# Performance work log

Measured on AMD Instinct MI355X. Metric: run time of the kernel, lower is better.

The kernel has to match this reference:

```python
import jax, jax.numpy as jnp
import numpy as np

HEADS = 8
HEAD_DIM = 32
SCALE = HEAD_DIM ** (-0.5)


def setup_inputs() -> dict:
    key = jax.random.key(0)
    k1, k2, k3 = jax.random.split(key, 3)
    B, DIM, N = 4, 512, 2048
    INNER = HEADS * HEAD_DIM  # 256
    x = jax.random.normal(k1, (B, DIM, N), dtype=jnp.float32)
    # Conv1d(kernel=1, bias=False) == channel-mixing matmul; weight (out_ch, in_ch)
    w_qkv = jax.random.normal(k2, (3 * INNER, DIM), dtype=jnp.float32) * (DIM ** -0.5)
    w_out = jax.random.normal(k3, (DIM, INNER), dtype=jnp.float32) * (INNER ** -0.5)
    b_out = jnp.zeros((DIM,), dtype=jnp.float32)
    return {"x": x, "w_qkv": w_qkv, "w_out": w_out, "b_out": b_out}


def reference(x, w_qkv, w_out, b_out):
    B, DIM, N = x.shape
    INNER = HEADS * HEAD_DIM
    # to_qkv: 1x1 conv over channels, then permute(0,2,1) -> (B, N, 3*INNER)
    qkv = jnp.einsum('bcn,oc->bno', x, w_qkv)
    q, k, v = jnp.split(qkv, 3, axis=-1)
    # 'b n (h d) -> b h n d'
    def to_heads(t):
        return t.reshape(B, N, HEADS, HEAD_DIM).transpose(0, 2, 1, 3)
    q, k, v = to_heads(q), to_heads(k), to_heads(v)
    # L2 similarity: -||q_i - k_j||_2 * scale, via expansion (avoids O(N^2 d) tensor)
    q2 = jnp.sum(q * q, axis=-1)            # (B,H,N)
    k2 = jnp.sum(k * k, axis=-1)            # (B,H,N)
    qk = jnp.einsum('bhid,bhjd->bhij', q, k)  # (B,H,N,N)
    dist2 = q2[..., :, None] + k2[..., None, :] - 2.0 * qk
    smi = -jnp.sqrt(jnp.maximum(dist2, 1e-12)) * SCALE
    attn = jax.nn.softmax(smi, axis=-1)
    out = jnp.einsum('bhij,bhjd->bhid', attn, v)  # (B,H,N,d)
    # 'b h n d -> b (h d) n'
    out = out.transpose(0, 1, 3, 2).reshape(B, INNER, N)
    # to_out: 1x1 conv with bias
    return jnp.einsum('bcn,oc->bon', out, w_out) + b_out[None, :, None]
```

## Files before the change

### kernel.cpp

```cpp
#include <hip/hip_runtime.h>
#include <math.h>

#define N_SEQ 2048
#define DIMC 512
#define INNER 256
#define C2F (0.17677669529663687f * 1.4426950408889634f)
#define C2F2 (C2F * C2F)

typedef short bf16x8 __attribute__((ext_vector_type(8)));
typedef float f32x4 __attribute__((ext_vector_type(4)));


static __device__ __forceinline__ ushort f2bf(float f) {
    uint x = __float_as_uint(f);
    x += 0x7fff + ((x >> 16) & 1);
    return (ushort)(x >> 16);
}
static __device__ __forceinline__ float bf2f(ushort u) {
    return __uint_as_float(((uint)u) << 16);
}
static __device__ __forceinline__ float fast_exp2_neg(float x) {
    float r; asm("v_exp_f32 %0, -%1" : "=v"(r) : "v"(x)); return r;
}
static __device__ __forceinline__ float fast_sqrt(float x) {
    float r; asm("v_sqrt_f32 %0, %1" : "=v"(r) : "v"(x)); return r;
}

__global__ void xpose_cvt(const float* __restrict__ x, ushort* __restrict__ xt) {
    __shared__ __align__(16) ushort T[64][72];
    const int b = blockIdx.z;
    const int c0 = blockIdx.y * 64;
    const int n0 = blockIdx.x * 64;
    const int t = threadIdx.x;
    const int cl = t >> 4;
    const int n4 = (t & 15) * 4;
    const float* xb = x + ((size_t)b * DIMC + c0) * N_SEQ + n0;
#pragma unroll
    for (int cc = 0; cc < 4; ++cc) {
        const int c = cl + cc * 16;
        float4 v = *(const float4*)(xb + (size_t)c * N_SEQ + n4);
        T[n4 + 0][c] = f2bf(v.x);
        T[n4 + 1][c] = f2bf(v.y);
        T[n4 + 2][c] = f2bf(v.z);
        T[n4 + 3][c] = f2bf(v.w);
    }
    __syncthreads();
    const int nl = t >> 2;
    const int c16 = (t & 3) * 16;
    uint4 v0 = *(const uint4*)&T[nl][c16];
    uint4 v1 = *(const uint4*)&T[nl][c16 + 8];
    ushort* dst = xt + ((size_t)b * N_SEQ + n0 + nl) * DIMC + c0 + c16;
    *(uint4*)dst = v0;
    *(uint4*)(dst + 8) = v1;
}

__global__ void wcvt2(const float* __restrict__ wq, const float* __restrict__ wo,
                      ushort* __restrict__ wq16, ushort* __restrict__ wo16) {
    const int bid = blockIdx.x;
    if (bid < 384) {
        int i = (bid * 256 + threadIdx.x) * 4;
        float4 v = *(const float4*)(wq + i);
        ushort4 p;
        p.x = f2bf(v.x); p.y = f2bf(v.y); p.z = f2bf(v.z); p.w = f2bf(v.w);
        *(ushort4*)(wq16 + i) = p;
    } else {
        int i = ((bid - 384) * 256 + threadIdx.x) * 4;
        float4 v = *(const float4*)(wo + i);
        ushort4 p;
        p.x = f2bf(v.x); p.y = f2bf(v.y); p.z = f2bf(v.z); p.w = f2bf(v.w);
        *(ushort4*)(wo16 + i) = p;
    }
}

__global__ __launch_bounds__(256) void qkv_mfma(const ushort* __restrict__ xt,
        const ushort* __restrict__ w16, ushort* __restrict__ ws16) {
    __shared__ __align__(16) ushort Wls[4 * 520];
    __shared__ __align__(16) ushort Xls[4 * 520];
    const int b = blockIdx.z;
    const int o0 = blockIdx.y * 64;
    const int n0 = blockIdx.x * 64;
    const int t = threadIdx.x;
    const int l = t & 63, w = t >> 6;
    const int q15 = l & 15, g = l >> 4;
    f32x4 acc[4];
#pragma unroll
    for (int nn = 0; nn < 4; ++nn) acc[nn] = (f32x4){0.f, 0.f, 0.f, 0.f};
    const int srow = t >> 2, sg = t & 3;
    const ushort* wsrc = w16 + (size_t)(o0 + srow) * DIMC + sg * 8;
    const ushort* xsrc = xt + ((size_t)b * N_SEQ + n0 + srow) * DIMC + sg * 8;
    uint4 wreg = *(const uint4*)wsrc;
    uint4 xreg = *(const uint4*)xsrc;
    for (int k0 = 0; k0 < DIMC; k0 += 32) {
        __builtin_amdgcn_s_barrier();
        __builtin_amdgcn_sched_barrier(0);
        *(uint4*)(Wls + sg * 520 + srow * 8) = wreg;
        *(uint4*)(Xls + sg * 520 + srow * 8) = xreg;
        if (k0 + 32 < DIMC) {
            wreg = *(const uint4*)(wsrc + k0 + 32);
            xreg = *(const uint4*)(xsrc + k0 + 32);
        }
        asm volatile("s_waitcnt lgkmcnt(0)" ::: "memory");
        __builtin_amdgcn_s_barrier();
        __builtin_amdgcn_sched_barrier(0);
        bf16x8 af = *(const bf16x8*)(Wls + g * 520 + (16 * w + q15) * 8);
        __builtin_amdgcn_s_setprio(1);
#pragma unroll
        for (int nn = 0; nn < 4; ++nn) {
            bf16x8 bfr = *(const bf16x8*)(Xls + g * 520 + (16 * nn + q15) * 8);
            acc[nn] = __builtin_amdgcn_mfma_f32_16x16x32_bf16(af, bfr, acc[nn], 0, 0, 0);
        }
        __builtin_amdgcn_s_setprio(0);
    }
    const int oatom = o0 + 16 * w;
    const int t_idx = oatom >> 8;
    const int h = (oatom >> 5) & 7;
    const int bh = b * 8 + h;
    const int d0 = (oatom & 31) + 4 * g;
    if (t_idx < 2) {
        ushort* dst = ws16 + (size_t)t_idx * 2097152 + (size_t)bh * 65536
                      + (size_t)(d0 >> 3) * 16384 + (d0 & 7);
#pragma unroll
        for (int nn = 0; nn < 4; ++nn) {
            const int n_ = n0 + 16 * nn + q15;
            ushort4 p;
            p.x = f2bf(acc[nn][0]); p.y = f2bf(acc[nn][1]);
            p.z = f2bf(acc[nn][2]); p.w = f2bf(acc[nn][3]);
            *(ushort4*)(dst + (size_t)n_ * 8) = p;
        }
    } else {
        ushort* dst = ws16 + (size_t)4194304 + (size_t)bh * 65536;
#pragma unroll
        for (int nn = 0; nn < 4; ++nn) {
            const int n_ = n0 + 16 * nn + q15;
            ushort* dd = dst + (size_t)(n_ >> 3) * 256 + (n_ & 7);
            dd[(d0 + 0) * 8] = f2bf(acc[nn][0]);
            dd[(d0 + 1) * 8] = f2bf(acc[nn][1]);
            dd[(d0 + 2) * 8] = f2bf(acc[nn][2]);
            dd[(d0 + 3) * 8] = f2bf(acc[nn][3]);
        }
    }
}

__global__ void sq_kernel(const ushort* __restrict__ ws16, float* __restrict__ k2) {
    const int idx = blockIdx.x * 256 + threadIdx.x;
    const int bh = idx >> 11, n = idx & 2047;
    const ushort* base = ws16 + 2097152 + (size_t)bh * 65536 + (size_t)n * 8;
    float s = 0.f;
#pragma unroll
    for (int g = 0; g < 4; ++g) {
        uint4 v = *(const uint4*)(base + (size_t)g * 16384);
        uint a[4] = {v.x, v.y, v.z, v.w};
#pragma unroll
        for (int e = 0; e < 4; ++e) {
            float lo = bf2f((ushort)(a[e] & 0xffff));
            float hi = bf2f((ushort)(a[e] >> 16));
            s += lo * lo + hi * hi;
        }
    }
    k2[idx] = s * (float)C2F2;
}

static __device__ __forceinline__ void load_kf(const ushort* __restrict__ Kf,
                                               int jh, bf16x8 (&kf)[4]) {
#pragma unroll
    for (int k = 0; k < 4; ++k)
        kf[k] = *(const bf16x8*)(Kf + (size_t)(jh + 16 * k) * 8);
}

static __device__ __forceinline__ void compute_half(
        const bf16x8 (&kf)[4], const ushort* __restrict__ Vf,
        const float* __restrict__ k2p, int jbase, int half, float q2v,
        bf16x8 qf, bf16x8 onesv, f32x4 (&accO)[2], f32x4& accS,
        ushort* __restrict__ plane, int g) {
    float4 kk[4];
#pragma unroll
    for (int k = 0; k < 4; ++k)
        kk[k] = *(const float4*)(k2p + jbase + half * 64 + 16 * k);
    bf16x8 vfr[4];
#pragma unroll
    for (int jc = 0; jc < 2; ++jc) {
        const int cl = 4 * (2 * half + jc) + g;
        vfr[jc * 2 + 0] = *(const bf16x8*)(Vf + (size_t)jbase * 32 + cl * 256);
        vfr[jc * 2 + 1] = *(const bf16x8*)(Vf + (size_t)jbase * 32 + cl * 256 + 128);
    }
    const f32x4 zz = (f32x4){0.f, 0.f, 0.f, 0.f};
    f32x4 st[4];
    __builtin_amdgcn_s_setprio(1);
#pragma unroll
    for (int k = 0; k < 4; ++k)
        st[k] = __builtin_amdgcn_mfma_f32_16x16x32_bf16(kf[k], qf, zz, 0, 0, 0);
    __builtin_amdgcn_s_setprio(0);
#pragma unroll
    for (int k = 0; k < 4; ++k) {
        float ka[4] = {kk[k].x, kk[k].y, kk[k].z, kk[k].w};
        float pr[4];
#pragma unroll
        for (int r = 0; r < 4; ++r) {
            float a = q2v + ka[r];
            float d2 = fmaf(-2.f * (float)C2F2, st[k][r], a);
            pr[r] = fast_exp2_neg(fast_sqrt(fmaxf(d2, 1e-12f)));
        }
        uint pk0, pk1;
        asm("v_cvt_pk_bf16_f32 %0, %1, %2" : "=v"(pk0) : "v"(pr[0]), "v"(pr[1]));
        asm("v_cvt_pk_bf16_f32 %0, %1, %2" : "=v"(pk1) : "v"(pr[2]), "v"(pr[3]));
        uint2 pv; pv.x = pk0; pv.y = pk1;
        *(uint2*)(plane + 16 * (4 * half + k) + 4 * g) = pv;
    }
    __builtin_amdgcn_s_setprio(1);
#pragma unroll
    for (int jc = 0; jc < 2; ++jc) {
        bf16x8 pf = *(const bf16x8*)(plane + 32 * (2 * half + jc) + 8 * g);
        accO[0] = __builtin_amdgcn_mfma_f32_16x16x32_bf16(vfr[jc * 2 + 0], pf, accO[0], 0, 0, 0);
        accO[1] = __builtin_amdgcn_mfma_f32_16x16x32_bf16(vfr[jc * 2 + 1], pf, accO[1], 0, 0, 0);
        accS = __builtin_amdgcn_mfma_f32_16x16x32_bf16(onesv, pf, accS, 0, 0, 0);
    }
    __builtin_amdgcn_s_setprio(0);
}

__global__ __launch_bounds__(256, 4) void attn_kernel(
        const ushort* __restrict__ ws16, const float* __restrict__ k2g,
        ushort* __restrict__ att16) {
    __shared__ __align__(16) ushort Pls[4][16][140];
    const int bid = blockIdx.x;
    const int sw = (bid & 7) * 128 + (bid >> 3);
    const int q0 = (sw & 31) * 64;
    const int bh = sw >> 5;
    const int b = bh >> 3, h = bh & 7;
    const int tid = threadIdx.x;
    const int l = tid & 63;
    const int w = tid >> 6;
    const int q15 = l & 15;
    const int g = l >> 4;
    const int qrow = q0 + 16 * w + q15;

    const ushort* Qbh = ws16 + (size_t)bh * 65536;
    const ushort* Kf = ws16 + 2097152 + (size_t)bh * 65536
                       + (size_t)g * 16384 + (size_t)q15 * 8;
    const ushort* Vf = ws16 + 4194304 + (size_t)bh * 65536 + (size_t)q15 * 8;
    const float* k2p = k2g + (size_t)bh * 2048 + 4 * g;

    const bf16x8 qf = *(const bf16x8*)(Qbh + (size_t)g * 16384 + (size_t)qrow * 8);
    float q2l = 0.f;
#pragma unroll
    for (int e = 0; e < 8; ++e) {
        float qe = bf2f((ushort)qf[e]);
        q2l = fmaf(qe, qe, q2l);
    }
    q2l += __shfl_xor(q2l, 16);
    q2l += __shfl_xor(q2l, 32);
    const float q2v = q2l * (float)C2F2;

    bf16x8 onesv;
#pragma unroll
    for (int e = 0; e < 8; ++e) onesv[e] = (short)0x3F80;
    ushort* plane = &Pls[w][q15][0];

    f32x4 accO[2];
    accO[0] = (f32x4){0.f, 0.f, 0.f, 0.f};
    accO[1] = (f32x4){0.f, 0.f, 0.f, 0.f};
    f32x4 accS = (f32x4){0.f, 0.f, 0.f, 0.f};

    bf16x8 kfA[4], kfB[4];
    load_kf(Kf, 0, kfA);
    load_kf(Kf, 64, kfB);
#pragma unroll 1
    for (int t = 0; t < 16; ++t) {
        const int jb = t * 128;
        compute_half(kfA, Vf, k2p, jb, 0, q2v, qf, onesv, accO, accS, plane, g);
        load_kf(Kf, jb + 128, kfA);
        __builtin_amdgcn_sched_barrier(0);
        compute_half(kfB, Vf, k2p, jb, 1, q2v, qf, onesv, accO, accS, plane, g);
        load_kf(Kf, jb + 192, kfB);
        __builtin_amdgcn_sched_barrier(0);
    }

    const float invl = 1.f / accS[0];
    ushort* dst = att16 + ((size_t)(b * N_SEQ + qrow)) * INNER + h * 32 + 4 * g;
#pragma unroll
    for (int d = 0; d < 2; ++d) {
        ushort4 o;
        o.x = f2bf(accO[d][0] * invl); o.y = f2bf(accO[d][1] * invl);
        o.z = f2bf(accO[d][2] * invl); o.w = f2bf(accO[d][3] * invl);
        *(ushort4*)(dst + d * 16) = o;
    }
}

__global__ __launch_bounds__(256) void out_mfma(const ushort* __restrict__ att16,
        const ushort* __restrict__ wo16, const float* __restrict__ bias,
        float* __restrict__ out) {
    __shared__ __align__(16) ushort Wls[4 * 520];
    __shared__ __align__(16) ushort Als[4 * 520];
    const int b = blockIdx.z;
    const int o0 = blockIdx.y * 64;
    const int n0 = blockIdx.x * 64;
    const int t = threadIdx.x;
    const int l = t & 63, w = t >> 6;
    const int q15 = l & 15, g = l >> 4;
    f32x4 acc[4];
#pragma unroll
    for (int nn = 0; nn < 4; ++nn) acc[nn] = (f32x4){0.f, 0.f, 0.f, 0.f};
    const int srow = t >> 2, sg = t & 3;
    const ushort* wsrc = wo16 + (size_t)(o0 + srow) * INNER + sg * 8;
    const ushort* asrc = att16 + ((size_t)b * N_SEQ + n0 + srow) * INNER + sg * 8;
    uint4 wreg = *(const uint4*)wsrc;
    uint4 areg = *(const uint4*)asrc;
    for (int k0 = 0; k0 < INNER; k0 += 32) {
        __builtin_amdgcn_s_barrier();
        __builtin_amdgcn_sched_barrier(0);
        *(uint4*)(Wls + sg * 520 + srow * 8) = wreg;
        *(uint4*)(Als + sg * 520 + srow * 8) = areg;
        if (k0 + 32 < INNER) {
            wreg = *(const uint4*)(wsrc + k0 + 32);
            areg = *(const uint4*)(asrc + k0 + 32);
        }
        asm volatile("s_waitcnt lgkmcnt(0)" ::: "memory");
        __builtin_amdgcn_s_barrier();
        __builtin_amdgcn_sched_barrier(0);
        bf16x8 af = *(const bf16x8*)(Wls + g * 520 + (16 * w + q15) * 8);
        __builtin_amdgcn_s_setprio(1);
#pragma unroll
        for (int nn = 0; nn < 4; ++nn) {
            bf16x8 bfr = *(const bf16x8*)(Als + g * 520 + (16 * nn + q15) * 8);
            acc[nn] = __builtin_amdgcn_mfma_f32_16x16x32_bf16(af, bfr, acc[nn], 0, 0, 0);
        }
        __builtin_amdgcn_s_setprio(0);
    }
    const int obase = o0 + 16 * w + 4 * g;
    float4 bi = *(const float4*)(bias + obase);
    float* ob = out + ((size_t)b * DIMC + obase) * N_SEQ;
#pragma unroll
    for (int nn = 0; nn < 4; ++nn) {
        const int n_ = n0 + 16 * nn + q15;
        ob[0 * N_SEQ + n_] = acc[nn][0] + bi.x;
        ob[1 * N_SEQ + n_] = acc[nn][1] + bi.y;
        ob[2 * N_SEQ + n_] = acc[nn][2] + bi.z;
        ob[3 * N_SEQ + n_] = acc[nn][3] + bi.w;
    }
}

extern "C" void kernel_launch(void* const* d_in, const int* in_sizes, int n_in,
                              void* d_out, int out_size, void* d_ws, size_t ws_size,
                              hipStream_t stream) {
    const float* x = (const float*)d_in[0];
    const float* w_qkv = (const float*)d_in[1];
    const float* w_out = (const float*)d_in[2];
    const float* b_out = (const float*)d_in[3];
    ushort* ws16 = (ushort*)d_ws;
    float* k2f = (float*)((char*)d_ws + (12 << 20) + (256 << 10));
    ushort* att16 = (ushort*)((char*)d_ws + (13 << 20));
    ushort* xt16 = (ushort*)((char*)d_ws + (21 << 20));
    ushort* wq16 = (ushort*)((char*)d_ws + (29 << 20));
    ushort* wo16 = (ushort*)((char*)d_ws + (30 << 20));
    float* out = (float*)d_out;

    xpose_cvt<<<dim3(32, 8, 4), 256, 0, stream>>>(x, xt16);
    wcvt2<<<dim3(512), 256, 0, stream>>>(w_qkv, w_out, wq16, wo16);
    qkv_mfma<<<dim3(32, 12, 4), 256, 0, stream>>>(xt16, wq16, ws16);
    sq_kernel<<<dim3(256), 256, 0, stream>>>(ws16, k2f);
    attn_kernel<<<dim3(1024), 256, 0, stream>>>(ws16, k2f, att16);
    out_mfma<<<dim3(32, 8, 4), 256, 0, stream>>>(att16, wo16, b_out, out);
}
```

Before: 91.51 us.

## Software-pipeline QK MFMA one step ahead and compute row sums on VALU

Restructures the attention inner loop so the QK^T MFMAs for the next 64-key chunk are issued while the current chunk's softmax weights are computed and multiplied with V, overlapping matrix and vector work. The softmax denominator is now accumulated in fp32 with VALU adds plus two cross-lane shuffles at the end. This replaces the extra ones-vector MFMA per P-tile. It increases register pressure (next-step st, double-buffered k2 values) and drops the explicit sched barriers. The denominator now sums fp32 weights instead of bf16-rounded ones, so it no longer matches exactly the weights used for P·V.

```diff
diff --git a/kernel.cpp b/kernel.cpp
--- a/kernel.cpp
+++ b/kernel.cpp
@@ -160,63 +160,6 @@
     k2[idx] = s * (float)C2F2;
 }
 
-static __device__ __forceinline__ void load_kf(const ushort* __restrict__ Kf,
-                                               int jh, bf16x8 (&kf)[4]) {
-#pragma unroll
-    for (int k = 0; k < 4; ++k)
-        kf[k] = *(const bf16x8*)(Kf + (size_t)(jh + 16 * k) * 8);
-}
-
-static __device__ __forceinline__ void compute_half(
-        const bf16x8 (&kf)[4], const ushort* __restrict__ Vf,
-        const float* __restrict__ k2p, int jbase, int half, float q2v,
-        bf16x8 qf, bf16x8 onesv, f32x4 (&accO)[2], f32x4& accS,
-        ushort* __restrict__ plane, int g) {
-    float4 kk[4];
-#pragma unroll
-    for (int k = 0; k < 4; ++k)
-        kk[k] = *(const float4*)(k2p + jbase + half * 64 + 16 * k);
-    bf16x8 vfr[4];
-#pragma unroll
-    for (int jc = 0; jc < 2; ++jc) {
-        const int cl = 4 * (2 * half + jc) + g;
-        vfr[jc * 2 + 0] = *(const bf16x8*)(Vf + (size_t)jbase * 32 + cl * 256);
-        vfr[jc * 2 + 1] = *(const bf16x8*)(Vf + (size_t)jbase * 32 + cl * 256 + 128);
-    }
-    const f32x4 zz = (f32x4){0.f, 0.f, 0.f, 0.f};
-    f32x4 st[4];
-    __builtin_amdgcn_s_setprio(1);
-#pragma unroll
-    for (int k = 0; k < 4; ++k)
-        st[k] = __builtin_amdgcn_mfma_f32_16x16x32_bf16(kf[k], qf, zz, 0, 0, 0);
-    __builtin_amdgcn_s_setprio(0);
-#pragma unroll
-    for (int k = 0; k < 4; ++k) {
-        float ka[4] = {kk[k].x, kk[k].y, kk[k].z, kk[k].w};
-        float pr[4];
-#pragma unroll
-        for (int r = 0; r < 4; ++r) {
-            float a = q2v + ka[r];
-            float d2 = fmaf(-2.f * (float)C2F2, st[k][r], a);
-            pr[r] = fast_exp2_neg(fast_sqrt(fmaxf(d2, 1e-12f)));
-        }
-        uint pk0, pk1;
-        asm("v_cvt_pk_bf16_f32 %0, %1, %2" : "=v"(pk0) : "v"(pr[0]), "v"(pr[1]));
-        asm("v_cvt_pk_bf16_f32 %0, %1, %2" : "=v"(pk1) : "v"(pr[2]), "v"(pr[3]));
-        uint2 pv; pv.x = pk0; pv.y = pk1;
-        *(uint2*)(plane + 16 * (4 * half + k) + 4 * g) = pv;
-    }
-    __builtin_amdgcn_s_setprio(1);
-#pragma unroll
-    for (int jc = 0; jc < 2; ++jc) {
-        bf16x8 pf = *(const bf16x8*)(plane + 32 * (2 * half + jc) + 8 * g);
-        accO[0] = __builtin_amdgcn_mfma_f32_16x16x32_bf16(vfr[jc * 2 + 0], pf, accO[0], 0, 0, 0);
-        accO[1] = __builtin_amdgcn_mfma_f32_16x16x32_bf16(vfr[jc * 2 + 1], pf, accO[1], 0, 0, 0);
-        accS = __builtin_amdgcn_mfma_f32_16x16x32_bf16(onesv, pf, accS, 0, 0, 0);
-    }
-    __builtin_amdgcn_s_setprio(0);
-}
-
 __global__ __launch_bounds__(256, 4) void attn_kernel(
         const ushort* __restrict__ ws16, const float* __restrict__ k2g,
         ushort* __restrict__ att16) {
@@ -250,31 +193,89 @@
     q2l += __shfl_xor(q2l, 32);
     const float q2v = q2l * (float)C2F2;
 
-    bf16x8 onesv;
-#pragma unroll
-    for (int e = 0; e < 8; ++e) onesv[e] = (short)0x3F80;
     ushort* plane = &Pls[w][q15][0];
-
     f32x4 accO[2];
     accO[0] = (f32x4){0.f, 0.f, 0.f, 0.f};
     accO[1] = (f32x4){0.f, 0.f, 0.f, 0.f};
-    f32x4 accS = (f32x4){0.f, 0.f, 0.f, 0.f};
-
-    bf16x8 kfA[4], kfB[4];
-    load_kf(Kf, 0, kfA);
-    load_kf(Kf, 64, kfB);
+    float lsm = 0.f;
+
+    f32x4 st[4];
+    bf16x8 kf[4];
+    float4 kkA[4], kkB[4];
+
+#pragma unroll
+    for (int k = 0; k < 4; ++k) kkA[k] = *(const float4*)(k2p + 16 * k);
+#pragma unroll
+    for (int k = 0; k < 4; ++k) kf[k] = *(const bf16x8*)(Kf + (size_t)(16 * k) * 8);
+    {
+        const f32x4 zz = (f32x4){0.f, 0.f, 0.f, 0.f};
+#pragma unroll
+        for (int k = 0; k < 4; ++k)
+            st[k] = __builtin_amdgcn_mfma_f32_16x16x32_bf16(kf[k], qf, zz, 0, 0, 0);
+    }
+
+#define ATTN_ITER(H, KKC, KKN)                                                  \
+    {                                                                           \
+        const int jb = (H) * 64;                                                \
+        const int hp = (H) & 1;                                                 \
+        bf16x8 vfr[4];                                                          \
+        _Pragma("unroll")                                                       \
+        for (int jc = 0; jc < 2; ++jc) {                                        \
+            const int c = 8 * (H) + 4 * jc + g;                                 \
+            vfr[jc * 2 + 0] = *(const bf16x8*)(Vf + (size_t)c * 256);           \
+            vfr[jc * 2 + 1] = *(const bf16x8*)(Vf + (size_t)c * 256 + 128);     \
+        }                                                                       \
+        _Pragma("unroll")                                                       \
+        for (int k = 0; k < 4; ++k)                                             \
+            KKN[k] = *(const float4*)(k2p + jb + 64 + 16 * k);                  \
+        _Pragma("unroll")                                                       \
+        for (int k = 0; k < 4; ++k)                                             \
+            kf[k] = *(const bf16x8*)(Kf + (size_t)(jb + 64 + 16 * k) * 8);      \
+        float lt = 0.f;                                                         \
+        _Pragma("unroll")                                                       \
+        for (int k = 0; k < 4; ++k) {                                           \
+            float ka[4] = {KKC[k].x, KKC[k].y, KKC[k].z, KKC[k].w};             \
+            float pr[4];                                                        \
+            _Pragma("unroll")                                                   \
+            for (int r = 0; r < 4; ++r) {                                       \
+                float a = q2v + ka[r];                                          \
+                float d2 = fmaf(-2.f * (float)C2F2, st[k][r], a);               \
+                pr[r] = fast_exp2_neg(fast_sqrt(fmaxf(d2, 1e-12f)));            \
+            }                                                                   \
+            lt += (pr[0] + pr[1]) + (pr[2] + pr[3]);                            \
+            uint pk0, pk1;                                                      \
+            asm("v_cvt_pk_bf16_f32 %0, %1, %2" : "=v"(pk0) : "v"(pr[0]), "v"(pr[1])); \
+            asm("v_cvt_pk_bf16_f32 %0, %1, %2" : "=v"(pk1) : "v"(pr[2]), "v"(pr[3])); \
+            uint2 pv; pv.x = pk0; pv.y = pk1;                                   \
+            *(uint2*)(plane + 16 * (4 * hp + k) + 4 * g) = pv;                  \
+        }                                                                       \
+        lsm += lt;                                                              \
+        const f32x4 zz = (f32x4){0.f, 0.f, 0.f, 0.f};                           \
+        __builtin_amdgcn_s_setprio(1);                                          \
+        _Pragma("unroll")                                                       \
+        for (int k = 0; k < 4; ++k)                                             \
+            st[k] = __builtin_amdgcn_mfma_f32_16x16x32_bf16(kf[k], qf, zz, 0, 0, 0); \
+        __builtin_amdgcn_s_setprio(0);                                          \
+        __builtin_amdgcn_s_setprio(1);                                          \
+        _Pragma("unroll")                                                       \
+        for (int jc = 0; jc < 2; ++jc) {                                        \
+            bf16x8 pf = *(const bf16x8*)(plane + 32 * (2 * hp + jc) + 8 * g);   \
+            accO[0] = __builtin_amdgcn_mfma_f32_16x16x32_bf16(vfr[jc * 2 + 0], pf, accO[0], 0, 0, 0); \
+            accO[1] = __builtin_amdgcn_mfma_f32_16x16x32_bf16(vfr[jc * 2 + 1], pf, accO[1], 0, 0, 0); \
+        }                                                                       \
+        __builtin_amdgcn_s_setprio(0);                                          \
+    }
+
 #pragma unroll 1
-    for (int t = 0; t < 16; ++t) {
-        const int jb = t * 128;
-        compute_half(kfA, Vf, k2p, jb, 0, q2v, qf, onesv, accO, accS, plane, g);
-        load_kf(Kf, jb + 128, kfA);
-        __builtin_amdgcn_sched_barrier(0);
-        compute_half(kfB, Vf, k2p, jb, 1, q2v, qf, onesv, accO, accS, plane, g);
-        load_kf(Kf, jb + 192, kfB);
-        __builtin_amdgcn_sched_barrier(0);
-    }
-
-    const float invl = 1.f / accS[0];
+    for (int hh = 0; hh < 32; hh += 2) {
+        ATTN_ITER(hh, kkA, kkB)
+        ATTN_ITER(hh + 1, kkB, kkA)
+    }
+#undef ATTN_ITER
+
+    lsm += __shfl_xor(lsm, 16);
+    lsm += __shfl_xor(lsm, 32);
+    const float invl = 1.f / lsm;
     ushort* dst = att16 + ((size_t)(b * N_SEQ + qrow)) * INNER + h * 32 + 4 * g;
 #pragma unroll
     for (int d = 0; d < 2; ++d) {
```

Measured after the change: 90.76 us. No clear change (-0.8%).
